# Kernel optimization log

Measured on AMD Instinct MI355X. Metric: run time of the kernel, lower is better.

The kernel has to match this reference:

```python
import jax, jax.numpy as jnp
import numpy as np
from jax import lax

C = 128
HEADS = 8
HID = 256  # int(C * 2.0)
B, H, W = 8, 128, 128
EPS_LN = 1e-5
EPS_NORM = 1e-12


def _dwconv(x, w, pad):
    # x: [B,C,H,W], w: [C,1,kh,kw] depthwise
    return lax.conv_general_dilated(
        x, w, window_strides=(1, 1), padding=[(pad, pad), (pad, pad)],
        dimension_numbers=("NCHW", "OIHW", "NCHW"), feature_group_count=x.shape[1])


def _conv1x1(x, w):
    # w: [O, I] pointwise conv
    return jnp.einsum("oi,bihw->bohw", w, x)


def _layernorm_c(x, gamma, beta):
    # torch: reshape to [B, HW, C], LayerNorm over C, reshape back == LN over channel axis
    mu = jnp.mean(x, axis=1, keepdims=True)
    var = jnp.mean(jnp.square(x - mu), axis=1, keepdims=True)
    xn = (x - mu) * lax.rsqrt(var + EPS_LN)
    return xn * gamma[None, :, None, None] + beta[None, :, None, None]


def _l2norm(x):
    n = jnp.sqrt(jnp.sum(jnp.square(x), axis=-1, keepdims=True))
    return x / jnp.maximum(n, EPS_NORM)


def _mdta(x, qkv_w, qkv_dw, temperature, attn_proj):
    b, c, h, w = x.shape
    qkv = _dwconv(_conv1x1(x, qkv_w), qkv_dw, pad=1)  # [B,3C,H,W]
    q, k, v = jnp.split(qkv, 3, axis=1)
    hd = c // HEADS
    q = q.reshape(b, HEADS, hd, h * w)
    k = k.reshape(b, HEADS, hd, h * w)
    v = v.reshape(b, HEADS, hd, h * w)
    q, k = _l2norm(q), _l2norm(k)
    attn = jax.nn.softmax(jnp.einsum("bhdn,bhen->bhde", q, k) * temperature, axis=-1)
    out = jnp.einsum("bhde,bhen->bhdn", attn, v).reshape(b, c, h, w)
    return _conv1x1(out, attn_proj)


def _gdfn2(x, pin_w, c1_w, c3_w, c5_w, pout_w):
    x = _conv1x1(x, pin_w)  # [B,HID,H,W]
    x1 = x * c1_w[None, :, 0, 0, 0, None, None]  # depthwise 1x1 == per-channel scale
    x3 = _dwconv(x, c3_w, pad=1)
    x5 = _dwconv(x, c5_w, pad=2)
    g = jax.nn.gelu(x1, approximate=False)
    gated = jnp.concatenate([g * x3, g * x5], axis=1)  # [B,2*HID,H,W]
    return _conv1x1(gated, pout_w)


def setup_inputs() -> dict:
    key = jax.random.key(0)
    ks = jax.random.split(key, 12)
    s = 0.05
    return {
        "x": jax.random.normal(ks[0], (B, C, H, W), jnp.float32),
        "ln1_w": jnp.ones((C,), jnp.float32),
        "ln1_b": jnp.zeros((C,), jnp.float32),
        "qkv_w": jax.random.normal(ks[1], (3 * C, C), jnp.float32) * s,
        "qkv_dw": jax.random.normal(ks[2], (3 * C, 1, 3, 3), jnp.float32) * s,
        "temperature": jnp.ones((1, HEADS, 1, 1), jnp.float32),
        "attn_proj": jax.random.normal(ks[3], (C, C), jnp.float32) * s,
        "ln2_w": jnp.ones((C,), jnp.float32),
        "ln2_b": jnp.zeros((C,), jnp.float32),
        "pin_w": jax.random.normal(ks[4], (HID, C), jnp.float32) * s,
        "c1_w": jax.random.normal(ks[5], (HID, 1, 1, 1), jnp.float32) * s,
        "c3_w": jax.random.normal(ks[6], (HID, 1, 3, 3), jnp.float32) * s,
        "c5_w": jax.random.normal(ks[7], (HID, 1, 5, 5), jnp.float32) * s,
        "pout_w": jax.random.normal(ks[8], (C, 2 * HID), jnp.float32) * s,
    }


def reference(x, ln1_w, ln1_b, qkv_w, qkv_dw, temperature, attn_proj,
              ln2_w, ln2_b, pin_w, c1_w, c3_w, c5_w, pout_w):
    x = x + _mdta(_layernorm_c(x, ln1_w, ln1_b), qkv_w, qkv_dw, temperature, attn_proj)
    x = x + _gdfn2(_layernorm_c(x, ln2_w, ln2_b), pin_w, c1_w, c3_w, c5_w, pout_w)
    return x
```

## Files before the change

### kernel.cpp

```cpp
#include <hip/hip_runtime.h>
#include <type_traits>

typedef unsigned short ushort;
typedef unsigned int uint;
typedef __bf16 bf16x8 __attribute__((ext_vector_type(8)));
typedef unsigned short ushort8v __attribute__((ext_vector_type(8)));
typedef float f32x4 __attribute__((ext_vector_type(4)));

__device__ __forceinline__ float b2f(ushort u) {
    unsigned int x = ((unsigned int)u) << 16;
    float f;
    __builtin_memcpy(&f, &x, 4);
    return f;
}
__device__ __forceinline__ ushort f2bf(float f) {
    unsigned int x;
    __builtin_memcpy(&x, &f, 4);
    unsigned int r = x + 0x7fffu + ((x >> 16) & 1u);
    return (ushort)(r >> 16);
}
__device__ __forceinline__ float u2f_lo(uint u) {
    uint x = u << 16;
    float f;
    __builtin_memcpy(&f, &x, 4);
    return f;
}
__device__ __forceinline__ float u2f_hi(uint u) {
    uint x = u & 0xffff0000u;
    float f;
    __builtin_memcpy(&f, &x, 4);
    return f;
}
__device__ __forceinline__ uint packbf(float a, float b) {
    return (uint)f2bf(a) | ((uint)f2bf(b) << 16);
}

#define NPIX 16384
#define PSTRIDE 136

__device__ __forceinline__ size_t tadr(int b, int CH, int tile, int ch, int off) {
    return (((size_t)b * 256 + tile) * CH + ch) * 64 + off;
}
__device__ __forceinline__ size_t padr(int b, int tile, int p, int c) {
    return (((size_t)b * 256 + tile) * 64 + p) * 128 + c;
}

__device__ __forceinline__ void stage_plane(ushort* pl, const ushort* __restrict__ src,
                                            int b, int c, int CH, int tid) {
    uint* plu = (uint*)pl;
    for (int i = tid; i < 784; i += 256) {
        int idx;
        if (i < 136) idx = i;
        else if (i < 272) idx = 8840 + (i - 136);
        else {
            int j = i - 272;
            int r = (j >> 2) + 2;
            int cs = j & 3;
            idx = r * 68 + (cs == 0 ? 0 : 64 + cs);
        }
        plu[idx] = 0u;
    }
    for (int i = tid; i < 2048; i += 256) {
        int row = i >> 4, xg = (i & 15) << 3;
        int px0 = row * 128 + xg;
        uint4 v = *(const uint4*)&src[tadr(b, CH, px0 >> 6, c, px0 & 63)];
        uint* dst = (uint*)&pl[(row + 2) * PSTRIDE + xg + 2];
        dst[0] = v.x; dst[1] = v.y; dst[2] = v.z; dst[3] = v.w;
    }
    __syncthreads();
}

__device__ __forceinline__ void unpack12(const ushort* rowp, float* cc) {
    const uint* rp = (const uint*)rowp;
    uint4 u = *(const uint4*)rp;
    uint2 v = *(const uint2*)(rp + 4);
    cc[0] = u2f_lo(u.x); cc[1] = u2f_hi(u.x);
    cc[2] = u2f_lo(u.y); cc[3] = u2f_hi(u.y);
    cc[4] = u2f_lo(u.z); cc[5] = u2f_hi(u.z);
    cc[6] = u2f_lo(u.w); cc[7] = u2f_hi(u.w);
    cc[8] = u2f_lo(v.x); cc[9] = u2f_hi(v.x);
    cc[10] = u2f_lo(v.y); cc[11] = u2f_hi(v.y);
}

__global__ __launch_bounds__(256) void wcvt(const float* __restrict__ s0, ushort* __restrict__ d0, int n0,
                                            const float* __restrict__ s1, ushort* __restrict__ d1, int n1,
                                            const float* __restrict__ s2, ushort* __restrict__ d2, int n2) {
    int i = blockIdx.x * 256 + threadIdx.x;
    if (i < n0) d0[i] = f2bf(s0[i]);
    else if (i < n0 + n1) d1[i - n0] = f2bf(s1[i - n0]);
    else if (i < n0 + n1 + n2) d2[i - n0 - n1] = f2bf(s2[i - n0 - n1]);
}

template <int O>
__global__ __launch_bounds__(256) void ln_gemm_mfma(const float* __restrict__ xin,
                                                    const ushort* __restrict__ Wb,
                                                    const float* __restrict__ gamma,
                                                    const float* __restrict__ beta,
                                                    ushort* __restrict__ out) {
    __shared__ ushort xs[64][136];
    __shared__ float red[2][4][64];
    __shared__ float mu[64], rs[64];
    __shared__ float gl[128], bl[128];

    const int blk = blockIdx.x;
    const int b = blk >> 8;
    const int tile = blk & 255;
    const int tid = threadIdx.x;

    const float* xb = xin + (size_t)b * 128 * NPIX + tile * 64;
    float vx[4][8];
#pragma unroll
    for (int k = 0; k < 4; k++) {
        int i = tid + k * 256;
        int p = i & 63, cg = i >> 6;
        const float* src = xb + (size_t)(cg * 8) * NPIX + p;
#pragma unroll
        for (int j = 0; j < 8; j++) vx[k][j] = src[(size_t)j * NPIX];
    }
    if (tid < 128) {
        gl[tid] = gamma[tid];
        bl[tid] = beta[tid];
    }
#pragma unroll
    for (int k = 0; k < 4; k++) {
        int i = tid + k * 256;
        int p = i & 63, cg = i >> 6;
        ushort8v u;
#pragma unroll
        for (int j = 0; j < 8; j++) u[j] = f2bf(vx[k][j]);
        *(ushort8v*)&xs[p][cg * 8] = u;
    }
    __syncthreads();

    {
        const int p = tid & 63, part = tid >> 6;
        float s = 0.f, ss = 0.f;
#pragma unroll
        for (int q = 0; q < 4; q++) {
            ushort8v u = *(const ushort8v*)&xs[p][part * 32 + q * 8];
#pragma unroll
            for (int j = 0; j < 8; j++) {
                float v = b2f(u[j]);
                s += v;
                ss += v * v;
            }
        }
        red[0][part][p] = s;
        red[1][part][p] = ss;
    }
    __syncthreads();
    if (tid < 64) {
        float s = red[0][0][tid] + red[0][1][tid] + red[0][2][tid] + red[0][3][tid];
        float ss = red[1][0][tid] + red[1][1][tid] + red[1][2][tid] + red[1][3][tid];
        float m = s * (1.f / 128.f);
        float var = ss * (1.f / 128.f) - m * m;
        mu[tid] = m;
        rs[tid] = rsqrtf(var + 1e-5f);
    }
    __syncthreads();
    {
        const int p = tid & 63, part = tid >> 6;
        const float mp = mu[p], rp = rs[p];
#pragma unroll
        for (int q = 0; q < 4; q++) {
            int c0 = part * 32 + q * 8;
            ushort8v u = *(const ushort8v*)&xs[p][c0];
            ushort8v o;
#pragma unroll
            for (int j = 0; j < 8; j++) {
                float v = b2f(u[j]);
                o[j] = f2bf((v - mp) * rp * gl[c0 + j] + bl[c0 + j]);
            }
            *(ushort8v*)&xs[p][c0] = o;
        }
    }
    __syncthreads();

    const int wv = tid >> 6, lane = tid & 63;
    const int lr = lane & 15, lg = lane >> 4;

    bf16x8 bfr[4][4];
#pragma unroll
    for (int t = 0; t < 4; t++)
#pragma unroll
        for (int kc = 0; kc < 4; kc++)
            bfr[t][kc] = __builtin_bit_cast(bf16x8, *(const ushort8v*)&xs[t * 16 + lr][kc * 32 + lg * 8]);

    constexpr int MT = O / 64;
    bf16x8 afp[2][4];
#pragma unroll
    for (int kc = 0; kc < 4; kc++)
        afp[0][kc] = __builtin_bit_cast(bf16x8,
            *(const ushort8v*)&Wb[(size_t)(wv * 16 + lr) * 128 + kc * 32 + lg * 8]);

    f32x4 accPair[2][4];
    const int rc = tid & 127, rhalf = tid >> 7;
    const int px8 = tid & 7, cb = tid >> 3;
    ushort* outp = out + tadr(b, O, tile, 0, 0);

#pragma unroll
    for (int mt = 0; mt < MT; mt++) {
        if (mt + 1 < MT) {
            const int o0n = ((mt + 1) * 4 + wv) * 16;
#pragma unroll
            for (int kc = 0; kc < 4; kc++)
                afp[(mt + 1) & 1][kc] = __builtin_bit_cast(bf16x8,
                    *(const ushort8v*)&Wb[(size_t)(o0n + lr) * 128 + kc * 32 + lg * 8]);
        }
        f32x4* acc = accPair[mt & 1];
#pragma unroll
        for (int t = 0; t < 4; t++) acc[t] = (f32x4){0.f, 0.f, 0.f, 0.f};
#pragma unroll
        for (int kc = 0; kc < 4; kc++)
#pragma unroll
            for (int t = 0; t < 4; t++)
                acc[t] = __builtin_amdgcn_mfma_f32_16x16x32_bf16(afp[mt & 1][kc], bfr[t][kc], acc[t], 0, 0, 0);

        if (mt & 1) {
            __syncthreads();
#pragma unroll
            for (int h = 0; h < 2; h++) {
                const int lc = h * 64 + wv * 16 + lg * 4;
#pragma unroll
                for (int t = 0; t < 4; t++) {
                    int px = t * 16 + lr;
                    uint2 pk;
                    pk.x = packbf(accPair[h][t][0], accPair[h][t][1]);
                    pk.y = packbf(accPair[h][t][2], accPair[h][t][3]);
                    *(uint2*)&xs[px][lc] = pk;
                }
            }
            __syncthreads();
            const int pairbase = (mt >> 1) * 128;
#pragma unroll
            for (int cc = 0; cc < 4; cc++) {
                int c = cb + cc * 32;
                ushort8v u;
#pragma unroll
                for (int j = 0; j < 8; j++) u[j] = xs[px8 * 8 + j][c];
                *(ushort8v*)&outp[(size_t)(pairbase + c) * 64 + px8 * 8] = u;
            }
        }
    }
    (void)rc; (void)rhalf;
}

__global__ __launch_bounds__(256) void dwconv3_lds(const ushort* __restrict__ in,
                                                   const float* __restrict__ wdw,
                                                   ushort* __restrict__ out, int CH) {
    __shared__ ushort pl[132 * PSTRIDE];
    const int c = blockIdx.x;
    const int b = blockIdx.y;
    const int tid = threadIdx.x;

    float w[9];
#pragma unroll
    for (int j = 0; j < 9; j++) w[j] = wdw[c * 9 + j];

    stage_plane(pl, in, b, c, CH, tid);

    const int x = (tid & 15) * 8;
    const int ybase = tid >> 4;
#pragma unroll 1
    for (int k = 0; k < 8; k++) {
        const int y = k * 16 + ybase;
        float a[8];
#pragma unroll
        for (int p = 0; p < 8; p++) a[p] = 0.f;
#pragma unroll
        for (int ky = 0; ky < 3; ky++) {
            float cc[12];
            unpack12(&pl[(y + ky + 1) * PSTRIDE + x], cc);
#pragma unroll
            for (int kx = 0; kx < 3; kx++) {
                float wv = w[ky * 3 + kx];
#pragma unroll
                for (int p = 0; p < 8; p++) a[p] += cc[p + kx + 1] * wv;
            }
        }
        const int px0 = (y << 7) + x;
        uint4 o;
        o.x = packbf(a[0], a[1]);
        o.y = packbf(a[2], a[3]);
        o.z = packbf(a[4], a[5]);
        o.w = packbf(a[6], a[7]);
        *(uint4*)&out[tadr(b, CH, px0 >> 6, c, px0 & 63)] = o;
    }
}

__global__ __launch_bounds__(256) void dw_gated(const ushort* __restrict__ t,
                                                const float* __restrict__ w3_,
                                                const float* __restrict__ w5_,
                                                const float* __restrict__ c1w,
                                                ushort* __restrict__ gated) {
    __shared__ ushort pl[132 * PSTRIDE];
    const int c = blockIdx.x;
    const int b = blockIdx.y;
    const int tid = threadIdx.x;

    float w3[9], w5[25];
#pragma unroll
    for (int j = 0; j < 9; j++) w3[j] = w3_[c * 9 + j];
#pragma unroll
    for (int j = 0; j < 25; j++) w5[j] = w5_[c * 25 + j];
    const float c1v = c1w[c];

    stage_plane(pl, t, b, c, 256, tid);

    const int x = (tid & 15) * 8;
    const int ybase = tid >> 4;
#pragma unroll 1
    for (int k = 0; k < 8; k++) {
        const int y = k * 16 + ybase;
        float a5[8], a3[8], tc[8];
#pragma unroll
        for (int p = 0; p < 8; p++) { a5[p] = 0.f; a3[p] = 0.f; }
#pragma unroll
        for (int ky = 0; ky < 5; ky++) {
            float cc[12];
            unpack12(&pl[(y + ky) * PSTRIDE + x], cc);
#pragma unroll
            for (int kx = 0; kx < 5; kx++) {
                float wv = w5[ky * 5 + kx];
#pragma unroll
                for (int p = 0; p < 8; p++) a5[p] += cc[p + kx] * wv;
            }
            if (ky >= 1 && ky <= 3) {
#pragma unroll
                for (int kx = 0; kx < 3; kx++) {
                    float wv = w3[(ky - 1) * 3 + kx];
#pragma unroll
                    for (int p = 0; p < 8; p++) a3[p] += cc[p + kx + 1] * wv;
                }
            }
            if (ky == 2) {
#pragma unroll
                for (int p = 0; p < 8; p++) tc[p] = cc[p + 2];
            }
        }
        const int px0 = (y << 7) + x;
        uint4 o3, o5;
        float g[8];
#pragma unroll
        for (int p = 0; p < 8; p++) {
            float x1 = tc[p] * c1v;
            g[p] = x1 * __builtin_amdgcn_rcpf(1.f + __expf(-1.702f * x1));
        }
        o3.x = packbf(g[0] * a3[0], g[1] * a3[1]);
        o3.y = packbf(g[2] * a3[2], g[3] * a3[3]);
        o3.z = packbf(g[4] * a3[4], g[5] * a3[5]);
        o3.w = packbf(g[6] * a3[6], g[7] * a3[7]);
        o5.x = packbf(g[0] * a5[0], g[1] * a5[1]);
        o5.y = packbf(g[2] * a5[2], g[3] * a5[3]);
        o5.z = packbf(g[4] * a5[4], g[5] * a5[5]);
        o5.w = packbf(g[6] * a5[6], g[7] * a5[7]);
        *(uint4*)&gated[tadr(b, 512, px0 >> 6, c, px0 & 63)] = o3;
        *(uint4*)&gated[tadr(b, 512, px0 >> 6, 256 + c, px0 & 63)] = o5;
    }
}

__global__ __launch_bounds__(256) void attn_M(const ushort* __restrict__ qkv,
                                              const float* __restrict__ temp,
                                              const float* __restrict__ attn_proj,
                                              ushort* __restrict__ M) {
    __shared__ float Sp[4][16][16];
    __shared__ float QSS[4][16], KSS[4][16];
    __shared__ float A[16][17];

    const int bh = blockIdx.x, b = bh >> 3, h = bh & 7;
    const int tid = threadIdx.x;
    const int w = tid >> 6, lane = tid & 63;
    const int lr = lane & 15, lg = lane >> 4;

    const size_t qbase = (((size_t)b * 256 + w * 64) * 384 + h * 16 + lr) * 64 + lg * 8;
    const size_t kbase = qbase + (size_t)128 * 64;

    f32x4 acc = {0.f, 0.f, 0.f, 0.f};
    f32x4 accq = {0.f, 0.f, 0.f, 0.f};
    f32x4 acck = {0.f, 0.f, 0.f, 0.f};
#pragma unroll 2
    for (int it = 0; it < 128; it++) {
        size_t off = (size_t)(it >> 1) * (384 * 64) + (it & 1) * 32;
        bf16x8 qf = __builtin_bit_cast(bf16x8, *(const ushort8v*)(qkv + qbase + off));
        bf16x8 kf = __builtin_bit_cast(bf16x8, *(const ushort8v*)(qkv + kbase + off));
        acc = __builtin_amdgcn_mfma_f32_16x16x32_bf16(qf, kf, acc, 0, 0, 0);
        accq = __builtin_amdgcn_mfma_f32_16x16x32_bf16(qf, qf, accq, 0, 0, 0);
        acck = __builtin_amdgcn_mfma_f32_16x16x32_bf16(kf, kf, acck, 0, 0, 0);
    }
#pragma unroll
    for (int r = 0; r < 4; r++) Sp[w][lg * 4 + r][lr] = acc[r];
    if (lg == (lr >> 2)) {
        QSS[w][lr] = accq[lr & 3];
        KSS[w][lr] = acck[lr & 3];
    }
    __syncthreads();

    const int d = tid >> 4, e = tid & 15;
    float S = Sp[0][d][e] + Sp[1][d][e] + Sp[2][d][e] + Sp[3][d][e];
    float nq = fmaxf(sqrtf(QSS[0][d] + QSS[1][d] + QSS[2][d] + QSS[3][d]), 1e-12f);
    float nk = fmaxf(sqrtf(KSS[0][e] + KSS[1][e] + KSS[2][e] + KSS[3][e]), 1e-12f);
    float logit = S / (nq * nk) * temp[h];
    float m = logit;
    for (int off = 8; off; off >>= 1) m = fmaxf(m, __shfl_xor(m, off, 64));
    float ex = expf(logit - m);
    float sum = ex;
    for (int off = 8; off; off >>= 1) sum += __shfl_xor(sum, off, 64);
    A[d][e] = ex / sum;
    __syncthreads();

    for (int i = tid; i < 2048; i += 256) {
        int o = i >> 4, ee = i & 15;
        float acc2 = 0.f;
#pragma unroll
        for (int dd = 0; dd < 16; dd++) acc2 += attn_proj[o * 128 + h * 16 + dd] * A[dd][ee];
        M[((size_t)b * 128 + o) * 128 + h * 16 + ee] = f2bf(acc2);
    }
}

__global__ __launch_bounds__(256) void mv_ln_mfma(const ushort* __restrict__ qkv,
                                                  const ushort* __restrict__ Mb16,
                                                  const float* __restrict__ x,
                                                  const ushort* __restrict__ pin_b,
                                                  const float* __restrict__ gamma,
                                                  const float* __restrict__ beta,
                                                  ushort* __restrict__ x2,
                                                  ushort* __restrict__ t_out) {
    __shared__ ushort vs[64][136];
    __shared__ ushort xs[64][136];
    __shared__ float red[2][4][64];
    __shared__ float mu[64], rs[64];
    __shared__ float gl[128], bl[128];

    const int blk = blockIdx.x;
    const int b = blk >> 8;
    const int tile = blk & 255;
    const int tid = threadIdx.x;
    const int wv = tid >> 6, lane = tid & 63;
    const int lr = lane & 15, lg = lane >> 4;

    const ushort* Mb = Mb16 + (size_t)b * 128 * 128;
    bf16x8 mfr[2][4];
#pragma unroll
    for (int mt = 0; mt < 2; mt++)
#pragma unroll
        for (int kc = 0; kc < 4; kc++)
            mfr[mt][kc] = __builtin_bit_cast(bf16x8,
                *(const ushort8v*)&Mb[(size_t)((wv * 2 + mt) * 16 + lr) * 128 + kc * 32 + lg * 8]);

    const ushort* vb = qkv + tadr(b, 384, tile, 256, 0);
    ushort8v vv[4];
#pragma unroll
    for (int k = 0; k < 4; k++) {
        int idx = tid + k * 256;
        int c = idx & 127, pg = idx >> 7;
        vv[k] = *(const ushort8v*)&vb[c * 64 + pg * 8];
    }
    if (tid < 128) {
        gl[tid] = gamma[tid];
        bl[tid] = beta[tid];
    }
#pragma unroll
    for (int k = 0; k < 4; k++) {
        int idx = tid + k * 256;
        int c = idx & 127, pg = idx >> 7;
#pragma unroll
        for (int j = 0; j < 8; j++) vs[pg * 8 + j][c] = vv[k][j];
    }
    __syncthreads();

    bf16x8 bfr[4][4];
#pragma unroll
    for (int t = 0; t < 4; t++)
#pragma unroll
        for (int kc = 0; kc < 4; kc++)
            bfr[t][kc] = __builtin_bit_cast(bf16x8, *(const ushort8v*)&vs[t * 16 + lr][kc * 32 + lg * 8]);

#pragma unroll
    for (int mt = 0; mt < 2; mt++) {
        const int o0 = (wv * 2 + mt) * 16;
        f32x4 acc[4] = {{0.f, 0.f, 0.f, 0.f}, {0.f, 0.f, 0.f, 0.f}, {0.f, 0.f, 0.f, 0.f}, {0.f, 0.f, 0.f, 0.f}};
#pragma unroll
        for (int kc = 0; kc < 4; kc++)
#pragma unroll
            for (int t = 0; t < 4; t++)
                acc[t] = __builtin_amdgcn_mfma_f32_16x16x32_bf16(mfr[mt][kc], bfr[t][kc], acc[t], 0, 0, 0);
#pragma unroll
        for (int t = 0; t < 4; t++) {
            int px = t * 16 + lr;
            const float* xp = &x[((size_t)b * 128 + o0 + lg * 4) * NPIX + tile * 64 + px];
            uint2 pk;
            pk.x = packbf(xp[0] + acc[t][0], xp[NPIX] + acc[t][1]);
            pk.y = packbf(xp[2 * NPIX] + acc[t][2], xp[3 * NPIX] + acc[t][3]);
            *(uint2*)&xs[px][o0 + lg * 4] = pk;
        }
    }

    bf16x8 pfp[2][4];
#pragma unroll
    for (int kc = 0; kc < 4; kc++)
        pfp[0][kc] = __builtin_bit_cast(bf16x8,
            *(const ushort8v*)&pin_b[(size_t)(wv * 16 + lr) * 128 + kc * 32 + lg * 8]);
    __syncthreads();

#pragma unroll
    for (int k = 0; k < 4; k++) {
        int idx = tid + k * 256;
        int p = idx >> 4, seg = idx & 15;
        uint4 v = *(const uint4*)&xs[p][seg * 8];
        *(uint4*)&x2[padr(b, tile, p, seg * 8)] = v;
    }
    {
        const int p = tid & 63, part = tid >> 6;
        float s = 0.f, ss = 0.f;
#pragma unroll
        for (int q = 0; q < 4; q++) {
            ushort8v u = *(const ushort8v*)&xs[p][part * 32 + q * 8];
#pragma unroll
            for (int j = 0; j < 8; j++) {
                float v = b2f(u[j]);
                s += v;
                ss += v * v;
            }
        }
        red[0][part][p] = s;
        red[1][part][p] = ss;
    }
    __syncthreads();
    if (tid < 64) {
        float s = red[0][0][tid] + red[0][1][tid] + red[0][2][tid] + red[0][3][tid];
        float ss = red[1][0][tid] + red[1][1][tid] + red[1][2][tid] + red[1][3][tid];
        float m = s * (1.f / 128.f);
        float var = ss * (1.f / 128.f) - m * m;
        mu[tid] = m;
        rs[tid] = rsqrtf(var + 1e-5f);
    }
    __syncthreads();
    {
        const int p = tid & 63, part = tid >> 6;
        const float mp = mu[p], rp = rs[p];
#pragma unroll
        for (int q = 0; q < 4; q++) {
            int c0 = part * 32 + q * 8;
            ushort8v u = *(const ushort8v*)&xs[p][c0];
            ushort8v o;
#pragma unroll
            for (int j = 0; j < 8; j++) {
                float v = b2f(u[j]);
                o[j] = f2bf((v - mp) * rp * gl[c0 + j] + bl[c0 + j]);
            }
            *(ushort8v*)&xs[p][c0] = o;
        }
    }
    __syncthreads();

    bf16x8 bfr2[4][4];
#pragma unroll
    for (int t = 0; t < 4; t++)
#pragma unroll
        for (int kc = 0; kc < 4; kc++)
            bfr2[t][kc] = __builtin_bit_cast(bf16x8, *(const ushort8v*)&xs[t * 16 + lr][kc * 32 + lg * 8]);

    f32x4 accPair[2][4];
    const int px8 = tid & 7, cb = tid >> 3;
    ushort* toutp = t_out + tadr(b, 256, tile, 0, 0);

#pragma unroll
    for (int mt = 0; mt < 4; mt++) {
        if (mt + 1 < 4) {
            const int o0n = ((mt + 1) * 4 + wv) * 16;
#pragma unroll
            for (int kc = 0; kc < 4; kc++)
                pfp[(mt + 1) & 1][kc] = __builtin_bit_cast(bf16x8,
                    *(const ushort8v*)&pin_b[(size_t)(o0n + lr) * 128 + kc * 32 + lg * 8]);
        }
        f32x4* acc = accPair[mt & 1];
#pragma unroll
        for (int t = 0; t < 4; t++) acc[t] = (f32x4){0.f, 0.f, 0.f, 0.f};
#pragma unroll
        for (int kc = 0; kc < 4; kc++)
#pragma unroll
            for (int t = 0; t < 4; t++)
                acc[t] = __builtin_amdgcn_mfma_f32_16x16x32_bf16(pfp[mt & 1][kc], bfr2[t][kc], acc[t], 0, 0, 0);

        if (mt & 1) {
            __syncthreads();
#pragma unroll
            for (int h = 0; h < 2; h++) {
                const int lc = h * 64 + wv * 16 + lg * 4;
#pragma unroll
                for (int t = 0; t < 4; t++) {
                    int px = t * 16 + lr;
                    uint2 pk;
                    pk.x = packbf(accPair[h][t][0], accPair[h][t][1]);
                    pk.y = packbf(accPair[h][t][2], accPair[h][t][3]);
                    *(uint2*)&vs[px][lc] = pk;
                }
            }
            __syncthreads();
            const int pairbase = (mt >> 1) * 128;
#pragma unroll
            for (int cc = 0; cc < 4; cc++) {
                int c = cb + cc * 32;
                ushort8v u;
#pragma unroll
                for (int j = 0; j < 8; j++) u[j] = vs[px8 * 8 + j][c];
                *(ushort8v*)&toutp[(size_t)(pairbase + c) * 64 + px8 * 8] = u;
            }
        }
    }
}

__global__ __launch_bounds__(256) void gdfn_mfma(const ushort* __restrict__ gated,
                                                 const ushort* __restrict__ x2,
                                                 const ushort* __restrict__ pout_b,
                                                 float* __restrict__ out) {
    __shared__ float smem[64 * 129];
    ushort (*gs)[64][72] = (ushort(*)[64][72])smem;
    float (*xf)[129] = (float(*)[129])smem;

    const int blk = blockIdx.x;
    const int b = blk >> 8;
    const int tile = blk & 255;
    const int tid = threadIdx.x;
    const int wv = tid >> 6, lane = tid & 63;
    const int lr = lane & 15, lg = lane >> 4;

    const ushort* gb = gated + tadr(b, 512, tile, 0, 0);
    const int p0 = tid & 63;
    const int kga = tid >> 6;

    f32x4 acc[2][4];
#pragma unroll
    for (int mt = 0; mt < 2; mt++)
#pragma unroll
        for (int tt = 0; tt < 4; tt++) acc[mt][tt] = (f32x4){0.f, 0.f, 0.f, 0.f};

    {
        ushort ca[8], cbv[8];
#pragma unroll
        for (int j = 0; j < 8; j++) ca[j] = gb[(kga * 8 + j) * 64 + p0];
#pragma unroll
        for (int j = 0; j < 8; j++) cbv[j] = gb[((kga + 4) * 8 + j) * 64 + p0];
        ushort8v ua, ub;
#pragma unroll
        for (int j = 0; j < 8; j++) { ua[j] = ca[j]; ub[j] = cbv[j]; }
        *(ushort8v*)&gs[0][p0][kga * 8] = ua;
        *(ushort8v*)&gs[0][p0][(kga + 4) * 8] = ub;
    }
    __syncthreads();

#pragma unroll
    for (int kb = 0; kb < 8; kb++) {
        const int cur = kb & 1;

        ushort na[8], nb[8];
        if (kb < 7) {
            const ushort* nbp = gb + (kb + 1) * 4096;
#pragma unroll
            for (int j = 0; j < 8; j++) na[j] = nbp[(kga * 8 + j) * 64 + p0];
#pragma unroll
            for (int j = 0; j < 8; j++) nb[j] = nbp[((kga + 4) * 8 + j) * 64 + p0];
        }

        bf16x8 bfrg[4][2];
#pragma unroll
        for (int tt = 0; tt < 4; tt++)
#pragma unroll
            for (int kc = 0; kc < 2; kc++)
                bfrg[tt][kc] = __builtin_bit_cast(bf16x8, *(const ushort8v*)&gs[cur][tt * 16 + lr][kc * 32 + lg * 8]);

#pragma unroll
        for (int mt = 0; mt < 2; mt++) {
            const int o0 = (wv * 2 + mt) * 16;
            bf16x8 afr[2];
#pragma unroll
            for (int kc = 0; kc < 2; kc++)
                afr[kc] = __builtin_bit_cast(bf16x8,
                    *(const ushort8v*)&pout_b[(size_t)(o0 + lr) * 512 + kb * 64 + kc * 32 + lg * 8]);
#pragma unroll
            for (int kc = 0; kc < 2; kc++)
#pragma unroll
                for (int tt = 0; tt < 4; tt++)
                    acc[mt][tt] = __builtin_amdgcn_mfma_f32_16x16x32_bf16(afr[kc], bfrg[tt][kc], acc[mt][tt], 0, 0, 0);
        }

        if (kb < 7) {
            ushort8v ua, ub;
#pragma unroll
            for (int j = 0; j < 8; j++) { ua[j] = na[j]; ub[j] = nb[j]; }
            *(ushort8v*)&gs[cur ^ 1][p0][kga * 8] = ua;
            *(ushort8v*)&gs[cur ^ 1][p0][(kga + 4) * 8] = ub;
        }
        __syncthreads();
    }

#pragma unroll
    for (int mt = 0; mt < 2; mt++)
#pragma unroll
        for (int tt = 0; tt < 4; tt++) {
            int o0 = (wv * 2 + mt) * 16 + lg * 4;
            int px = tt * 16 + lr;
            uint2 xw = *(const uint2*)&x2[padr(b, tile, px, o0)];
            xf[px][o0 + 0] = u2f_lo(xw.x) + acc[mt][tt][0];
            xf[px][o0 + 1] = u2f_hi(xw.x) + acc[mt][tt][1];
            xf[px][o0 + 2] = u2f_lo(xw.y) + acc[mt][tt][2];
            xf[px][o0 + 3] = u2f_hi(xw.y) + acc[mt][tt][3];
        }
    __syncthreads();
    {
        const int qx = tid & 15;
        const int cbase = tid >> 4;
#pragma unroll
        for (int cc = 0; cc < 8; cc++) {
            int c = cbase + cc * 16;
            float4 v;
            v.x = xf[qx * 4 + 0][c];
            v.y = xf[qx * 4 + 1][c];
            v.z = xf[qx * 4 + 2][c];
            v.w = xf[qx * 4 + 3][c];
            *(float4*)&out[((size_t)b * 128 + c) * NPIX + tile * 64 + qx * 4] = v;
        }
    }
}

extern "C" void kernel_launch(void* const* d_in, const int* in_sizes, int n_in,
                              void* d_out, int out_size, void* d_ws, size_t ws_size,
                              hipStream_t stream) {
    const float* x = (const float*)d_in[0];
    const float* ln1_w = (const float*)d_in[1];
    const float* ln1_b = (const float*)d_in[2];
    const float* qkv_w = (const float*)d_in[3];
    const float* qkv_dw = (const float*)d_in[4];
    const float* temperature = (const float*)d_in[5];
    const float* attn_proj = (const float*)d_in[6];
    const float* ln2_w = (const float*)d_in[7];
    const float* ln2_b = (const float*)d_in[8];
    const float* pin_w = (const float*)d_in[9];
    const float* c1_w = (const float*)d_in[10];
    const float* c3_w = (const float*)d_in[11];
    const float* c5_w = (const float*)d_in[12];
    const float* pout_w = (const float*)d_in[13];
    float* out = (float*)d_out;

    char* ws = (char*)d_ws;
    ushort* qkv_pre = (ushort*)(ws + 0);
    ushort* qkv     = (ushort*)(ws + 100663296);
    ushort* x2      = (ushort*)(ws + 201326592);
    ushort* t       = (ushort*)(ws + 0);
    ushort* gated   = (ushort*)(ws + 67108864);
    ushort* Mb16    = (ushort*)(ws + 235151360);
    ushort* qkv_wb  = (ushort*)(ws + 235413504);
    ushort* pin_wb  = (ushort*)(ws + 235511808);
    ushort* pout_wb = (ushort*)(ws + 235577344);

    wcvt<<<576, 256, 0, stream>>>(qkv_w, qkv_wb, 49152, pin_w, pin_wb, 32768, pout_w, pout_wb, 65536);
    ln_gemm_mfma<384><<<2048, 256, 0, stream>>>(x, qkv_wb, ln1_w, ln1_b, qkv_pre);
    dwconv3_lds<<<dim3(384, 8), 256, 0, stream>>>(qkv_pre, qkv_dw, qkv, 384);
    attn_M<<<64, 256, 0, stream>>>(qkv, temperature, attn_proj, Mb16);
    mv_ln_mfma<<<2048, 256, 0, stream>>>(qkv, Mb16, x, pin_wb, ln2_w, ln2_b, x2, t);
    dw_gated<<<dim3(256, 8), 256, 0, stream>>>(t, c3_w, c5_w, c1_w, gated);
    gdfn_mfma<<<2048, 256, 0, stream>>>(gated, x2, pout_wb, out);
}
```

Measured before the change: 302.9 us.

## Shrink LDS footprint in mv_ln and gdfn kernels, widen attn_M to 512 threads

attn_M now launches 512 threads per block, so eight waves each reduce half as many pixel groups and the partial sums are combined over eight slices. mv_ln_mfma merges its two LDS tiles into one buffer, with an extra barrier so the buffer can be reused safely. gdfn_mfma writes its fp32 epilogue in two 32-pixel halves, letting the transpose buffer shrink to the size of the double-buffered gate tile. The LDS savings aim to raise occupancy in the two large kernels, at the cost of extra barriers and serialized epilogue halves.

```diff
diff --git a/kernel.cpp b/kernel.cpp
--- a/kernel.cpp
+++ b/kernel.cpp
@@ -194,7 +194,6 @@
             *(const ushort8v*)&Wb[(size_t)(wv * 16 + lr) * 128 + kc * 32 + lg * 8]);
 
     f32x4 accPair[2][4];
-    const int rc = tid & 127, rhalf = tid >> 7;
     const int px8 = tid & 7, cb = tid >> 3;
     ushort* outp = out + tadr(b, O, tile, 0, 0);
 
@@ -242,7 +241,6 @@
             }
         }
     }
-    (void)rc; (void)rhalf;
 }
 
 __global__ __launch_bounds__(256) void dwconv3_lds(const ushort* __restrict__ in,
@@ -359,12 +357,12 @@
     }
 }
 
-__global__ __launch_bounds__(256) void attn_M(const ushort* __restrict__ qkv,
+__global__ __launch_bounds__(512) void attn_M(const ushort* __restrict__ qkv,
                                               const float* __restrict__ temp,
                                               const float* __restrict__ attn_proj,
                                               ushort* __restrict__ M) {
-    __shared__ float Sp[4][16][16];
-    __shared__ float QSS[4][16], KSS[4][16];
+    __shared__ float Sp[8][16][16];
+    __shared__ float QSS[8][16], KSS[8][16];
     __shared__ float A[16][17];
 
     const int bh = blockIdx.x, b = bh >> 3, h = bh & 7;
@@ -372,14 +370,14 @@
     const int w = tid >> 6, lane = tid & 63;
     const int lr = lane & 15, lg = lane >> 4;
 
-    const size_t qbase = (((size_t)b * 256 + w * 64) * 384 + h * 16 + lr) * 64 + lg * 8;
+    const size_t qbase = (((size_t)b * 256 + w * 32) * 384 + h * 16 + lr) * 64 + lg * 8;
     const size_t kbase = qbase + (size_t)128 * 64;
 
     f32x4 acc = {0.f, 0.f, 0.f, 0.f};
     f32x4 accq = {0.f, 0.f, 0.f, 0.f};
     f32x4 acck = {0.f, 0.f, 0.f, 0.f};
 #pragma unroll 2
-    for (int it = 0; it < 128; it++) {
+    for (int it = 0; it < 64; it++) {
         size_t off = (size_t)(it >> 1) * (384 * 64) + (it & 1) * 32;
         bf16x8 qf = __builtin_bit_cast(bf16x8, *(const ushort8v*)(qkv + qbase + off));
         bf16x8 kf = __builtin_bit_cast(bf16x8, *(const ushort8v*)(qkv + kbase + off));
@@ -395,20 +393,28 @@
     }
     __syncthreads();
 
-    const int d = tid >> 4, e = tid & 15;
-    float S = Sp[0][d][e] + Sp[1][d][e] + Sp[2][d][e] + Sp[3][d][e];
-    float nq = fmaxf(sqrtf(QSS[0][d] + QSS[1][d] + QSS[2][d] + QSS[3][d]), 1e-12f);
-    float nk = fmaxf(sqrtf(KSS[0][e] + KSS[1][e] + KSS[2][e] + KSS[3][e]), 1e-12f);
-    float logit = S / (nq * nk) * temp[h];
-    float m = logit;
-    for (int off = 8; off; off >>= 1) m = fmaxf(m, __shfl_xor(m, off, 64));
-    float ex = expf(logit - m);
-    float sum = ex;
-    for (int off = 8; off; off >>= 1) sum += __shfl_xor(sum, off, 64);
-    A[d][e] = ex / sum;
-    __syncthreads();
-
-    for (int i = tid; i < 2048; i += 256) {
+    if (tid < 256) {
+        const int d = tid >> 4, e = tid & 15;
+        float S = 0.f, q2 = 0.f, k2 = 0.f;
+#pragma unroll
+        for (int s = 0; s < 8; s++) {
+            S += Sp[s][d][e];
+            q2 += QSS[s][d];
+            k2 += KSS[s][e];
+        }
+        float nq = fmaxf(sqrtf(q2), 1e-12f);
+        float nk = fmaxf(sqrtf(k2), 1e-12f);
+        float logit = S / (nq * nk) * temp[h];
+        float m = logit;
+        for (int off = 8; off; off >>= 1) m = fmaxf(m, __shfl_xor(m, off, 64));
+        float ex = expf(logit - m);
+        float sum = ex;
+        for (int off = 8; off; off >>= 1) sum += __shfl_xor(sum, off, 64);
+        A[d][e] = ex / sum;
+    }
+    __syncthreads();
+
+    for (int i = tid; i < 2048; i += 512) {
         int o = i >> 4, ee = i & 15;
         float acc2 = 0.f;
 #pragma unroll
@@ -425,8 +431,7 @@
                                                   const float* __restrict__ beta,
                                                   ushort* __restrict__ x2,
                                                   ushort* __restrict__ t_out) {
-    __shared__ ushort vs[64][136];
-    __shared__ ushort xs[64][136];
+    __shared__ ushort ts[64][136];
     __shared__ float red[2][4][64];
     __shared__ float mu[64], rs[64];
     __shared__ float gl[128], bl[128];
@@ -464,7 +469,7 @@
         int idx = tid + k * 256;
         int c = idx & 127, pg = idx >> 7;
 #pragma unroll
-        for (int j = 0; j < 8; j++) vs[pg * 8 + j][c] = vv[k][j];
+        for (int j = 0; j < 8; j++) ts[pg * 8 + j][c] = vv[k][j];
     }
     __syncthreads();
 
@@ -473,7 +478,8 @@
     for (int t = 0; t < 4; t++)
 #pragma unroll
         for (int kc = 0; kc < 4; kc++)
-            bfr[t][kc] = __builtin_bit_cast(bf16x8, *(const ushort8v*)&vs[t * 16 + lr][kc * 32 + lg * 8]);
+            bfr[t][kc] = __builtin_bit_cast(bf16x8, *(const ushort8v*)&ts[t * 16 + lr][kc * 32 + lg * 8]);
+    __syncthreads();
 
 #pragma unroll
     for (int mt = 0; mt < 2; mt++) {
@@ -491,7 +497,7 @@
             uint2 pk;
             pk.x = packbf(xp[0] + acc[t][0], xp[NPIX] + acc[t][1]);
             pk.y = packbf(xp[2 * NPIX] + acc[t][2], xp[3 * NPIX] + acc[t][3]);
-            *(uint2*)&xs[px][o0 + lg * 4] = pk;
+            *(uint2*)&ts[px][o0 + lg * 4] = pk;
         }
     }
 
@@ -506,7 +512,7 @@
     for (int k = 0; k < 4; k++) {
         int idx = tid + k * 256;
         int p = idx >> 4, seg = idx & 15;
-        uint4 v = *(const uint4*)&xs[p][seg * 8];
+        uint4 v = *(const uint4*)&ts[p][seg * 8];
         *(uint4*)&x2[padr(b, tile, p, seg * 8)] = v;
     }
     {
@@ -514,7 +520,7 @@
         float s = 0.f, ss = 0.f;
 #pragma unroll
         for (int q = 0; q < 4; q++) {
-            ushort8v u = *(const ushort8v*)&xs[p][part * 32 + q * 8];
+            ushort8v u = *(const ushort8v*)&ts[p][part * 32 + q * 8];
 #pragma unroll
             for (int j = 0; j < 8; j++) {
                 float v = b2f(u[j]);
@@ -541,14 +547,14 @@
 #pragma unroll
         for (int q = 0; q < 4; q++) {
             int c0 = part * 32 + q * 8;
-            ushort8v u = *(const ushort8v*)&xs[p][c0];
+            ushort8v u = *(const ushort8v*)&ts[p][c0];
             ushort8v o;
 #pragma unroll
             for (int j = 0; j < 8; j++) {
                 float v = b2f(u[j]);
                 o[j] = f2bf((v - mp) * rp * gl[c0 + j] + bl[c0 + j]);
             }
-            *(ushort8v*)&xs[p][c0] = o;
+            *(ushort8v*)&ts[p][c0] = o;
         }
     }
     __syncthreads();
@@ -558,7 +564,7 @@
     for (int t = 0; t < 4; t++)
 #pragma unroll
         for (int kc = 0; kc < 4; kc++)
-            bfr2[t][kc] = __builtin_bit_cast(bf16x8, *(const ushort8v*)&xs[t * 16 + lr][kc * 32 + lg * 8]);
+            bfr2[t][kc] = __builtin_bit_cast(bf16x8, *(const ushort8v*)&ts[t * 16 + lr][kc * 32 + lg * 8]);
 
     f32x4 accPair[2][4];
     const int px8 = tid & 7, cb = tid >> 3;
@@ -593,7 +599,7 @@
                     uint2 pk;
                     pk.x = packbf(accPair[h][t][0], accPair[h][t][1]);
                     pk.y = packbf(accPair[h][t][2], accPair[h][t][3]);
-                    *(uint2*)&vs[px][lc] = pk;
+                    *(uint2*)&ts[px][lc] = pk;
                 }
             }
             __syncthreads();
@@ -603,7 +609,7 @@
                 int c = cb + cc * 32;
                 ushort8v u;
 #pragma unroll
-                for (int j = 0; j < 8; j++) u[j] = vs[px8 * 8 + j][c];
+                for (int j = 0; j < 8; j++) u[j] = ts[px8 * 8 + j][c];
                 *(ushort8v*)&toutp[(size_t)(pairbase + c) * 64 + px8 * 8] = u;
             }
         }
@@ -614,9 +620,8 @@
                                                  const ushort* __restrict__ x2,
                                                  const ushort* __restrict__ pout_b,
                                                  float* __restrict__ out) {
-    __shared__ float smem[64 * 129];
-    ushort (*gs)[64][72] = (ushort(*)[64][72])smem;
-    float (*xf)[129] = (float(*)[129])smem;
+    __shared__ ushort gs[2][64][72];
+    float (*xf)[129] = (float(*)[129])gs;
 
     const int blk = blockIdx.x;
     const int b = blk >> 8;
@@ -695,31 +700,36 @@
     }
 
 #pragma unroll
-    for (int mt = 0; mt < 2; mt++)
-#pragma unroll
-        for (int tt = 0; tt < 4; tt++) {
-            int o0 = (wv * 2 + mt) * 16 + lg * 4;
-            int px = tt * 16 + lr;
-            uint2 xw = *(const uint2*)&x2[padr(b, tile, px, o0)];
-            xf[px][o0 + 0] = u2f_lo(xw.x) + acc[mt][tt][0];
-            xf[px][o0 + 1] = u2f_hi(xw.x) + acc[mt][tt][1];
-            xf[px][o0 + 2] = u2f_lo(xw.y) + acc[mt][tt][2];
-            xf[px][o0 + 3] = u2f_hi(xw.y) + acc[mt][tt][3];
-        }
-    __syncthreads();
-    {
-        const int qx = tid & 15;
-        const int cbase = tid >> 4;
-#pragma unroll
-        for (int cc = 0; cc < 8; cc++) {
-            int c = cbase + cc * 16;
-            float4 v;
-            v.x = xf[qx * 4 + 0][c];
-            v.y = xf[qx * 4 + 1][c];
-            v.z = xf[qx * 4 + 2][c];
-            v.w = xf[qx * 4 + 3][c];
-            *(float4*)&out[((size_t)b * 128 + c) * NPIX + tile * 64 + qx * 4] = v;
-        }
+    for (int h = 0; h < 2; h++) {
+#pragma unroll
+        for (int mt = 0; mt < 2; mt++)
+#pragma unroll
+            for (int t2 = 0; t2 < 2; t2++) {
+                const int tt = h * 2 + t2;
+                int o0 = (wv * 2 + mt) * 16 + lg * 4;
+                int px = tt * 16 + lr;
+                uint2 xw = *(const uint2*)&x2[padr(b, tile, px, o0)];
+                xf[px - h * 32][o0 + 0] = u2f_lo(xw.x) + acc[mt][tt][0];
+                xf[px - h * 32][o0 + 1] = u2f_hi(xw.x) + acc[mt][tt][1];
+                xf[px - h * 32][o0 + 2] = u2f_lo(xw.y) + acc[mt][tt][2];
+                xf[px - h * 32][o0 + 3] = u2f_hi(xw.y) + acc[mt][tt][3];
+            }
+        __syncthreads();
+        {
+            const int qx = tid & 7;
+            const int cbase = tid >> 3;
+#pragma unroll
+            for (int cc = 0; cc < 4; cc++) {
+                int c = cbase + cc * 32;
+                float4 v;
+                v.x = xf[qx * 4 + 0][c];
+                v.y = xf[qx * 4 + 1][c];
+                v.z = xf[qx * 4 + 2][c];
+                v.w = xf[qx * 4 + 3][c];
+                *(float4*)&out[((size_t)b * 128 + c) * NPIX + tile * 64 + h * 32 + qx * 4] = v;
+            }
+        }
+        __syncthreads();
     }
 }
 
@@ -756,7 +766,7 @@
     wcvt<<<576, 256, 0, stream>>>(qkv_w, qkv_wb, 49152, pin_w, pin_wb, 32768, pout_w, pout_wb, 65536);
     ln_gemm_mfma<384><<<2048, 256, 0, stream>>>(x, qkv_wb, ln1_w, ln1_b, qkv_pre);
     dwconv3_lds<<<dim3(384, 8), 256, 0, stream>>>(qkv_pre, qkv_dw, qkv, 384);
-    attn_M<<<64, 256, 0, stream>>>(qkv, temperature, attn_proj, Mb16);
+    attn_M<<<64, 512, 0, stream>>>(qkv, temperature, attn_proj, Mb16);
     mv_ln_mfma<<<2048, 256, 0, stream>>>(qkv, Mb16, x, pin_wb, ln2_w, ln2_b, x2, t);
     dw_gated<<<dim3(256, 8), 256, 0, stream>>>(t, c3_w, c5_w, c1_w, gated);
     gdfn_mfma<<<2048, 256, 0, stream>>>(gated, x2, pout_wb, out);
```

After: 301.7 us. No clear change (-0.4%).
